# Optimization experiments

Measured on AMD Instinct MI355X. Metric: run time of the kernel, lower is better.

The kernel has to match this reference:

```python
import jax, jax.numpy as jnp
import numpy as np

BN_EPS = 1e-5


def _conv1d(x, w, b):
    # x: (B, C, T), w: (O, C, K), torch Conv1d with padding=K//2
    k = w.shape[-1]
    p = k // 2
    out = jax.lax.conv_general_dilated(
        x, w, window_strides=(1,), padding=[(p, p)],
        dimension_numbers=("NCH", "OIH", "NCH"))
    return out + b[None, :, None]


def setup_inputs() -> dict:
    key = jax.random.key(0)
    ks = jax.random.split(key, 16)
    B, C, T, H, NC = 32, 13, 2048, 128, 10
    d = {
        "x": jax.random.normal(ks[0], (B, C, T), jnp.float32),
        "w1": jax.random.normal(ks[1], (H, C, 10), jnp.float32) * 0.1,
        "b1": jax.random.normal(ks[2], (H,), jnp.float32) * 0.1,
        "w2": jax.random.normal(ks[3], (H, C, 20), jnp.float32) * 0.1,
        "b2": jax.random.normal(ks[4], (H,), jnp.float32) * 0.1,
        "w3": jax.random.normal(ks[5], (H, C, 30), jnp.float32) * 0.1,
        "b3": jax.random.normal(ks[6], (H,), jnp.float32) * 0.1,
        "w4": jax.random.normal(ks[7], (H, C, 40), jnp.float32) * 0.1,
        "b4": jax.random.normal(ks[8], (H,), jnp.float32) * 0.1,
        "bn_gamma": jax.random.uniform(ks[9], (4 * H,), jnp.float32, 0.5, 1.5),
        "bn_beta": jax.random.normal(ks[10], (4 * H,), jnp.float32) * 0.1,
        "bn_mean": jnp.zeros((4 * H,), jnp.float32),
        "bn_var": jnp.ones((4 * H,), jnp.float32),
        "logreg_w": jax.random.normal(ks[11], (NC, 4 * H), jnp.float32) * 0.05,
        "logreg_b": jax.random.normal(ks[12], (NC,), jnp.float32) * 0.1,
        "dec_w": jax.random.normal(ks[13], (1, 4 * H), jnp.float32) * 0.05,
        "dec_b": jax.random.normal(ks[14], (1,), jnp.float32) * 0.1,
    }
    return d


def reference(x, w1, b1, w2, b2, w3, b3, w4, b4,
              bn_gamma, bn_beta, bn_mean, bn_var,
              logreg_w, logreg_b, dec_w, dec_b):
    # --- multi-scale shapelet conv + per-prefix cumulative max pooling ---
    feats = []
    for w, b in ((w1, b1), (w2, b2), (w3, b3), (w4, b4)):
        f = _conv1d(x, w, b)                      # (B, H, T+1) (even kernels)
        # original loop: for t in 1..T_out-1 take max over f[:, :, :t]
        # == running (cumulative) max, dropping the last prefix
        cm = jax.lax.cummax(f, axis=2)[:, :, :-1]  # (B, H, T)
        feats.append(jnp.transpose(cm, (0, 2, 1)))  # (B, T, H)
    features = jnp.concatenate(feats, axis=-1)      # (B, T, 4H)

    # --- BatchNorm1d over feature channels (eval mode), dropout = identity ---
    inv = jax.lax.rsqrt(bn_var + BN_EPS)
    features = (features - bn_mean) * (inv * bn_gamma) + bn_beta

    # --- classification head and halting head ---
    logits = jnp.einsum("btf,cf->btc", features, logreg_w) + logreg_b  # (B,T,NC)
    deltas = jnp.einsum("btf,of->bto", features, dec_w) + dec_b        # (B,T,1)
    deltas = jax.nn.softmax(deltas[..., 0], axis=1)                    # (B,T)

    # --- attention budget: pt_t = delta_t * budget_{t-1}; budget decays ---
    B = deltas.shape[0]
    q = 1.0 - deltas                                # (B, T)
    cp = jnp.cumprod(q[:, 1:], axis=1)              # prod_{s=1..t} q_s
    budget = jnp.concatenate([jnp.ones((B, 1), deltas.dtype), cp], axis=1)
    pts_loop = deltas[:, 1:] * budget[:, :-1]       # (B, T-1)
    pts = jnp.concatenate([pts_loop, budget[:, -1:]], axis=1)  # (B, T)

    probs = jax.nn.softmax(logits, axis=-1)  # temperature = 1
    return probs, pts
```

## Files before the change

kernel.cpp:

```cpp
#include <hip/hip_runtime.h>
#include <math.h>

#define NEG_INF (-3.402823466e38f)

typedef float f32x4 __attribute__((ext_vector_type(4)));
typedef short bf16x8 __attribute__((ext_vector_type(8)));
typedef unsigned int u32x4 __attribute__((ext_vector_type(4)));

__device__ __forceinline__ unsigned short f2bf(float f) {
    unsigned int u = __float_as_uint(f);
    unsigned int r = (u + 0x7FFFu + ((u >> 16) & 1u)) >> 16;
    return (unsigned short)r;
}
__device__ __forceinline__ float bf2f(unsigned short s) {
    return __uint_as_float(((unsigned int)s) << 16);
}
__device__ __forceinline__ unsigned int pack2(float a, float b) {
    return (unsigned int)f2bf(a) | ((unsigned int)f2bf(b) << 16);
}
__device__ __forceinline__ int swz(int a) { return a ^ (((a >> 5) & 7) << 4); }

__global__ __launch_bounds__(512) void prep_kernel(
    const float* __restrict__ x,
    const float* __restrict__ w1, const float* __restrict__ w2,
    const float* __restrict__ w3, const float* __restrict__ w4,
    const float* __restrict__ bn_gamma, const float* __restrict__ bn_beta,
    const float* __restrict__ bn_mean, const float* __restrict__ bn_var,
    const float* __restrict__ lw, const float* __restrict__ lb,
    const float* __restrict__ dw, const float* __restrict__ db,
    unsigned short* __restrict__ xT, unsigned short* __restrict__ Bfrag,
    unsigned short* __restrict__ hfrag, float* __restrict__ bfo,
    float* __restrict__ dbfo)
{
    int bid = blockIdx.x;
    int tid = threadIdx.x;
    if (bid < 136) {
        int idx = bid * 512 + tid;
        int b = idx / 2176, r = idx - b * 2176;
        int t = r - 20;
        unsigned short row[16];
#pragma unroll
        for (int c = 0; c < 16; ++c) {
            float v = (c < 13 && t >= 0 && t < 2048) ? x[((size_t)(b * 13 + c)) * 2048 + t] : 0.f;
            row[c] = f2bf(v);
        }
        u32x4* dst = (u32x4*)(xT + (size_t)idx * 16);
        u32x4 v0, v1;
        v0.x = row[0] | ((unsigned)row[1] << 16);  v0.y = row[2] | ((unsigned)row[3] << 16);
        v0.z = row[4] | ((unsigned)row[5] << 16);  v0.w = row[6] | ((unsigned)row[7] << 16);
        v1.x = row[8] | ((unsigned)row[9] << 16);  v1.y = row[10] | ((unsigned)row[11] << 16);
        v1.z = row[12] | ((unsigned)row[13] << 16); v1.w = row[14] | ((unsigned)row[15] << 16);
        dst[0] = v0; dst[1] = v1;
    } else if (bid < 186) {
        int idx = (bid - 136) * 512 + tid;
        int lane = idx & 63, frag = idx >> 6;
        int rel, Kc; const float* w;
        if (frag < 40)       { rel = frag;       w = w1; Kc = 10; }
        else if (frag < 120) { rel = frag - 40;  w = w2; Kc = 20; }
        else if (frag < 240) { rel = frag - 120; w = w3; Kc = 30; }
        else                 { rel = frag - 240; w = w4; Kc = 40; }
        int kh = Kc / 2;
        int ht = rel / kh;
        int k0 = rel - ht * kh;
        int h = ht * 16 + (lane & 15);
        int dk = lane >> 5;
        int cbase = 8 * ((lane >> 4) & 1);
        int k = 2 * k0 + dk;
        unsigned short e[8];
#pragma unroll
        for (int j = 0; j < 8; ++j) {
            int c = cbase + j;
            float v = (c < 13) ? w[((size_t)h * 13 + c) * Kc + k] : 0.f;
            e[j] = f2bf(v);
        }
        u32x4 pk;
        pk.x = e[0] | ((unsigned)e[1] << 16); pk.y = e[2] | ((unsigned)e[3] << 16);
        pk.z = e[4] | ((unsigned)e[5] << 16); pk.w = e[6] | ((unsigned)e[7] << 16);
        *(u32x4*)(Bfrag + (size_t)frag * 512 + lane * 8) = pk;
    } else if (bid == 186) {
        __shared__ float sh[512];
        int j = tid;
        float s = rsqrtf(bn_var[j] + 1e-5f) * bn_gamma[j];
        float shift = bn_beta[j] - bn_mean[j] * s;
        sh[j] = shift;
        __syncthreads();
        if (j < 10) {
            float acc = lb[j];
            for (int q = 0; q < 512; ++q) acc += sh[q] * lw[j * 512 + q];
            bfo[j] = acc;
        } else if (j == 10) {
            float acc = db[0];
            for (int q = 0; q < 512; ++q) acc += sh[q] * dw[q];
            dbfo[0] = acc;
        }
    } else {
        int idx = (bid - 187) * 512 + tid;
        int lane = idx & 63, frag = idx >> 6;
        int n = lane & 15;
        unsigned short e[8];
#pragma unroll
        for (int jj = 0; jj < 8; ++jj) {
            int k = frag * 32 + 8 * (lane >> 4) + jj;
            float s = rsqrtf(bn_var[k] + 1e-5f) * bn_gamma[k];
            float v = (n < 10) ? lw[n * 512 + k] * s : (n == 10) ? dw[k] * s : 0.f;
            e[jj] = f2bf(v);
        }
        u32x4 pk;
        pk.x = e[0] | ((unsigned)e[1] << 16); pk.y = e[2] | ((unsigned)e[3] << 16);
        pk.z = e[4] | ((unsigned)e[5] << 16); pk.w = e[6] | ((unsigned)e[7] << 16);
        *(u32x4*)(hfrag + (size_t)frag * 512 + lane * 8) = pk;
    }
}

__global__ __launch_bounds__(256, 2) void conv_mfma(
    const unsigned short* __restrict__ xT, const unsigned short* __restrict__ Bfrag,
    const float* __restrict__ b1, const float* __restrict__ b2,
    const float* __restrict__ b3, const float* __restrict__ b4,
    unsigned short* __restrict__ feat, unsigned short* __restrict__ totals)
{
    __shared__ __align__(16) unsigned short lds[2688 + 2 * 32 * 132];
    unsigned short* xs = lds;
    unsigned int* stg32 = (unsigned int*)(lds + 2688);
    const int tid = threadIdx.x;
    const int tq = blockIdx.x & 15;
    const int scale = (blockIdx.x >> 4) & 3;
    const int b = blockIdx.x >> 6;
    const int kh_tab[4] = {5, 10, 15, 20};
    const int so_tab[4] = {0, 40, 120, 240};
    const int KH = kh_tab[scale];
    const int P = 5 * (scale + 1);
    const float* bias = (scale == 0) ? b1 : (scale == 1) ? b2 : (scale == 2) ? b3 : b4;

    const unsigned short* src = xT + ((size_t)b * 2176 + tq * 128) * 16;
#pragma unroll
    for (int it = 0; it < 2; ++it) {
        int c = it * 256 + tid;
        if (c < 336) {
            u32x4 v = *(const u32x4*)(src + c * 8);
            *(u32x4*)((char*)xs + swz(c * 16)) = v;
        }
    }
    __syncthreads();

    const int lane = tid & 63;
    const int wave = tid >> 6;
    const int hgrp = wave & 1;
    const int twq = wave >> 1;
    const int l15 = lane & 15;
    const int g4 = lane >> 4;

    const unsigned short* bfr = Bfrag + ((size_t)(so_tab[scale] + hgrp * 4 * KH)) * 512 + lane * 8;
    float bv[4];
#pragma unroll
    for (int ht = 0; ht < 4; ++ht) bv[ht] = bias[hgrp * 64 + ht * 16 + l15];

    int abase = ((20 - P) + twq * 64 + l15 + (lane >> 5)) * 32 + (g4 & 1) * 16;

    f32x4 acc[4][4];
#pragma unroll
    for (int ht = 0; ht < 4; ++ht)
#pragma unroll
        for (int tt = 0; tt < 4; ++tt)
            acc[ht][tt] = (f32x4){bv[ht], bv[ht], bv[ht], bv[ht]};

#define LOADB(DST, K) \
    _Pragma("unroll") for (int ht_ = 0; ht_ < 4; ++ht_) \
        DST[ht_] = *(const bf16x8*)(bfr + (size_t)(ht_ * KH + (K)) * 512);
#define LOADA(DST, K) \
    _Pragma("unroll") for (int tt_ = 0; tt_ < 4; ++tt_) \
        DST[tt_] = *(const bf16x8*)((const char*)xs + swz(abase + tt_ * 512 + (K) * 64));
#define MFMA16(AA, BB) \
    _Pragma("unroll") for (int ht_ = 0; ht_ < 4; ++ht_) \
        _Pragma("unroll") for (int tt_ = 0; tt_ < 4; ++tt_) \
            acc[ht_][tt_] = __builtin_amdgcn_mfma_f32_16x16x32_bf16(AA[tt_], BB[ht_], acc[ht_][tt_], 0, 0, 0);

    bf16x8 A0[4], A1[4], B0[4], B1[4];
    LOADB(B0, 0); LOADA(A0, 0);
    int k0 = 0;
#pragma unroll 1
    while (k0 + 2 <= KH) {
        LOADB(B1, k0 + 1); LOADA(A1, k0 + 1);
        MFMA16(A0, B0);
        if (k0 + 2 < KH) { LOADB(B0, k0 + 2); LOADA(A0, k0 + 2); }
        MFMA16(A1, B1);
        k0 += 2;
    }
    if (k0 < KH) { MFMA16(A0, B0); }
#undef LOADB
#undef LOADA
#undef MFMA16

    float carry[4] = {NEG_INF, NEG_INF, NEG_INF, NEG_INF};
    const int rq = tq * 2 + twq;
#pragma unroll
    for (int tt = 0; tt < 4; ++tt) {
#pragma unroll
        for (int ht = 0; ht < 4; ++ht) {
            f32x4 v = acc[ht][tt];
            float s0 = v.x;
            float s1 = fmaxf(v.y, s0);
            float s2 = fmaxf(v.z, s1);
            float s3 = fmaxf(v.w, s2);
            float inc = s3;
            float o = __shfl_up(inc, 16); if (lane >= 16) inc = fmaxf(inc, o);
            o = __shfl_up(inc, 32);       if (lane >= 32) inc = fmaxf(inc, o);
            float pre = __shfl_up(inc, 16);
            float base = (lane >= 16) ? fmaxf(carry[ht], pre) : carry[ht];
            s0 = fmaxf(s0, base); s1 = fmaxf(s1, base);
            s2 = fmaxf(s2, base); s3 = fmaxf(s3, base);
            float tot = __shfl(inc, l15 + 48);
            carry[ht] = fmaxf(carry[ht], tot);
            acc[ht][tt] = (f32x4){s0, s1, s2, s3};
        }
    }
    if (lane < 16) {
#pragma unroll
        for (int ht = 0; ht < 4; ++ht) {
            int j = scale * 128 + hgrp * 64 + ht * 16 + l15;
            totals[((size_t)b * 32 + rq) * 512 + j] = f2bf(carry[ht]);
        }
    }

#pragma unroll 1
    for (int half = 0; half < 2; ++half) {
        if (half) __syncthreads();
        if (twq == half) {
#pragma unroll
            for (int tt = 0; tt < 4; ++tt) {
#pragma unroll
                for (int ht = 0; ht < 4; ++ht) {
                    f32x4 s = acc[ht][tt];
                    int r2 = tt * 8 + 2 * g4;
                    int cc = hgrp * 64 + ht * 16 + l15;
                    stg32[r2 * 132 + cc]       = pack2(s.x, s.y);
                    stg32[(r2 + 1) * 132 + cc] = pack2(s.z, s.w);
                }
            }
        }
        __syncthreads();
        size_t grow = (size_t)b * 2048 + tq * 128 + half * 64;
#pragma unroll
        for (int i = 0; i < 2; ++i) {
            int e = i * 256 + tid;
            int r2 = e >> 4, q = e & 15;
            const unsigned int* p = stg32 + r2 * 132 + q * 8;
            u32x4 da = *(const u32x4*)(p);
            u32x4 dbb = *(const u32x4*)(p + 4);
            u32x4 ev, od;
            ev.x = (da.x & 0xffffu) | (da.y << 16);
            ev.y = (da.z & 0xffffu) | (da.w << 16);
            ev.z = (dbb.x & 0xffffu) | (dbb.y << 16);
            ev.w = (dbb.z & 0xffffu) | (dbb.w << 16);
            od.x = (da.x >> 16) | (da.y & 0xffff0000u);
            od.y = (da.z >> 16) | (da.w & 0xffff0000u);
            od.z = (dbb.x >> 16) | (dbb.y & 0xffff0000u);
            od.w = (dbb.z >> 16) | (dbb.w & 0xffff0000u);
            size_t base = (grow + 2 * r2) * 512 + scale * 128 + q * 8;
            __builtin_nontemporal_store(ev, (u32x4*)(feat + base));
            __builtin_nontemporal_store(od, (u32x4*)(feat + base + 512));
        }
    }
}

__global__ __launch_bounds__(256) void head_kernel(
    const unsigned short* __restrict__ feat, const unsigned short* __restrict__ totals,
    const unsigned short* __restrict__ hfrag, const float* __restrict__ bfo,
    const float* __restrict__ dbfo, float* __restrict__ probs,
    float* __restrict__ delta_raw)
{
    __shared__ float pfs[512];
    int b = blockIdx.x >> 5;
    int tc = blockIdx.x & 31;
    int tid = threadIdx.x;
    int lane = tid & 63;
    int wave = tid >> 6;

    for (int j = tid; j < 512; j += 256) {
        float run = NEG_INF;
        for (int qq = 0; qq < tc; ++qq)
            run = fmaxf(run, bf2f(totals[((size_t)b * 32 + qq) * 512 + j]));
        pfs[j] = run;
    }
    __syncthreads();

    bf16x8 Bf[16];
#pragma unroll
    for (int k0 = 0; k0 < 16; ++k0)
        Bf[k0] = *(const bf16x8*)(hfrag + (size_t)k0 * 512 + lane * 8);

    const int n = lane & 15;
    const int g4 = lane >> 4;
    const int tb = tc * 64 + wave * 16;
    const unsigned short* fb = feat + ((size_t)b * 2048 + tb + n) * 512 + 8 * g4;

    float biasv = (n < 10) ? bfo[n] : (n == 10) ? dbfo[0] : 0.f;
    f32x4 acc = (f32x4){biasv, biasv, biasv, biasv};

#pragma unroll
    for (int k0 = 0; k0 < 16; ++k0) {
        bf16x8 a = *(const bf16x8*)(fb + k0 * 32);
        const float* pp = pfs + k0 * 32 + 8 * g4;
        union { unsigned int u[4]; bf16x8 v; } aw;
#pragma unroll
        for (int i = 0; i < 4; ++i) {
            float lo = fmaxf(bf2f((unsigned short)a[2 * i]),     pp[2 * i]);
            float hi = fmaxf(bf2f((unsigned short)a[2 * i + 1]), pp[2 * i + 1]);
            aw.u[i] = (__float_as_uint(lo) >> 16) | (__float_as_uint(hi) & 0xFFFF0000u);
        }
        acc = __builtin_amdgcn_mfma_f32_16x16x32_bf16(aw.v, Bf[k0], acc, 0, 0, 0);
    }

#pragma unroll
    for (int r = 0; r < 4; ++r) {
        float v = acc[r];
        float vm = (n < 10) ? v : NEG_INF;
#pragma unroll
        for (int off = 1; off < 16; off <<= 1)
            vm = fmaxf(vm, __shfl_xor(vm, off, 16));
        float e = (n < 10) ? __expf(v - vm) : 0.f;
        float s = e;
#pragma unroll
        for (int off = 1; off < 16; off <<= 1)
            s += __shfl_xor(s, off, 16);
        int t = tb + g4 * 4 + r;
        if (n < 10) probs[((size_t)b * 2048 + t) * 10 + n] = e / s;
        if (n == 10) delta_raw[b * 2048 + t] = v;
    }
}

__global__ __launch_bounds__(256) void budget_kernel(
    const float* __restrict__ delta_raw, float* __restrict__ pts)
{
    __shared__ float ds[2048];
    __shared__ float red[8];
    int b = blockIdx.x;
    int tid = threadIdx.x;
    int lane = tid & 63, wid = tid >> 6;
    const float* row = delta_raw + b * 2048;
    int base = tid * 8;
    float d[8];
#pragma unroll
    for (int i = 0; i < 8; ++i) d[i] = row[base + i];
    float m = d[0];
#pragma unroll
    for (int i = 1; i < 8; ++i) m = fmaxf(m, d[i]);
#pragma unroll
    for (int off = 1; off < 64; off <<= 1) m = fmaxf(m, __shfl_xor(m, off));
    if (lane == 0) red[wid] = m;
    __syncthreads();
    m = fmaxf(fmaxf(red[0], red[1]), fmaxf(red[2], red[3]));
    float s = 0.f;
#pragma unroll
    for (int i = 0; i < 8; ++i) { d[i] = __expf(d[i] - m); s += d[i]; }
#pragma unroll
    for (int off = 1; off < 64; off <<= 1) s += __shfl_xor(s, off);
    if (lane == 0) red[4 + wid] = s;
    __syncthreads();
    float inv = 1.f / (red[4] + red[5] + red[6] + red[7]);
    float g[8], p = 1.f;
#pragma unroll
    for (int i = 0; i < 8; ++i) {
        d[i] *= inv;
        ds[base + i] = d[i];
        float gv = (base + i == 0) ? 1.f : (1.f - d[i]);
        p *= gv;
        g[i] = p;
    }
    float sp = p;
#pragma unroll
    for (int off = 1; off < 64; off <<= 1) {
        float o = __shfl_up(sp, off);
        if (lane >= off) sp *= o;
    }
    float pre_t = __shfl_up(sp, 1);
    if (lane == 0) pre_t = 1.f;
    if (lane == 63) red[wid] = sp;
    __syncthreads();
    float wpre = 1.f;
#pragma unroll
    for (int w = 0; w < 4; ++w) if (w < wid) wpre *= red[w];
    float pre = wpre * pre_t;
#pragma unroll
    for (int i = 0; i < 8; ++i) {
        int t = base + i;
        float budget = pre * g[i];
        float pt = (t < 2047) ? ds[t + 1] * budget : budget;
        pts[b * 2048 + t] = pt;
    }
}

extern "C" void kernel_launch(void* const* d_in, const int* in_sizes, int n_in,
                              void* d_out, int out_size, void* d_ws, size_t ws_size,
                              hipStream_t stream)
{
    const float* x     = (const float*)d_in[0];
    const float* w1    = (const float*)d_in[1];
    const float* b1    = (const float*)d_in[2];
    const float* w2    = (const float*)d_in[3];
    const float* b2    = (const float*)d_in[4];
    const float* w3    = (const float*)d_in[5];
    const float* b3    = (const float*)d_in[6];
    const float* w4    = (const float*)d_in[7];
    const float* b4    = (const float*)d_in[8];
    const float* gamma = (const float*)d_in[9];
    const float* beta  = (const float*)d_in[10];
    const float* mean  = (const float*)d_in[11];
    const float* var   = (const float*)d_in[12];
    const float* lw    = (const float*)d_in[13];
    const float* lb    = (const float*)d_in[14];
    const float* dw    = (const float*)d_in[15];
    const float* db    = (const float*)d_in[16];

    char* ws = (char*)d_ws;
    unsigned short* feat   = (unsigned short*)ws;
    unsigned short* xT     = (unsigned short*)(ws + 67108864);
    unsigned short* Bfrag  = (unsigned short*)(ws + 69337088);
    unsigned short* totals = (unsigned short*)(ws + 69746688);
    float* draw   = (float*)(ws + 70795264);
    unsigned short* hfrag = (unsigned short*)(ws + 71057408);
    float* bfo    = (float*)(ws + 71073792);
    float* dbfo   = (float*)(ws + 71073856);

    float* probs = (float*)d_out;
    float* pts   = probs + (size_t)32 * 2048 * 10;

    hipLaunchKernelGGL(prep_kernel, dim3(189), dim3(512), 0, stream,
                       x, w1, w2, w3, w4, gamma, beta, mean, var,
                       lw, lb, dw, db, xT, Bfrag, hfrag, bfo, dbfo);
    hipLaunchKernelGGL(conv_mfma, dim3(2048), dim3(256), 0, stream,
                       xT, Bfrag, b1, b2, b3, b4, feat, totals);
    hipLaunchKernelGGL(head_kernel, dim3(1024), dim3(256), 0, stream,
                       feat, totals, hfrag, bfo, dbfo, probs, draw);
    hipLaunchKernelGGL(budget_kernel, dim3(32), dim3(256), 0, stream, draw, pts);
}
```

Before: 89.10 us.

## Double conv tile to 256 timesteps per block with 8 MFMA tiles per wave

Each conv block now covers 256 timesteps instead of 128, so every wave holds 4x8 accumulator tiles and reuses each loaded B fragment across twice as many MFMAs, and the grid is halved. The x load now reads only the halo needed for the scale, and the software-pipelined double-buffered K loop becomes a simple loop. The cummax emits two per-64-row totals (mid and end), and the feature stores drop the nontemporal hint. Register pressure roughly doubles for the accumulators, which may reduce occupancy or spill under launch_bounds(256,2), and the simpler loop loses load/compute overlap.

```diff
diff --git a/kernel.cpp b/kernel.cpp
--- a/kernel.cpp
+++ b/kernel.cpp
@@ -118,24 +118,25 @@
     const float* __restrict__ b3, const float* __restrict__ b4,
     unsigned short* __restrict__ feat, unsigned short* __restrict__ totals)
 {
-    __shared__ __align__(16) unsigned short lds[2688 + 2 * 32 * 132];
+    __shared__ __align__(16) unsigned short lds[4736 + 16896];
     unsigned short* xs = lds;
-    unsigned int* stg32 = (unsigned int*)(lds + 2688);
+    unsigned int* stg32 = (unsigned int*)(lds + 4736);
     const int tid = threadIdx.x;
-    const int tq = blockIdx.x & 15;
-    const int scale = (blockIdx.x >> 4) & 3;
-    const int b = blockIdx.x >> 6;
+    const int tq = blockIdx.x & 7;
+    const int scale = (blockIdx.x >> 3) & 3;
+    const int b = blockIdx.x >> 5;
     const int kh_tab[4] = {5, 10, 15, 20};
     const int so_tab[4] = {0, 40, 120, 240};
     const int KH = kh_tab[scale];
     const int P = 5 * (scale + 1);
     const float* bias = (scale == 0) ? b1 : (scale == 1) ? b2 : (scale == 2) ? b3 : b4;
 
-    const unsigned short* src = xT + ((size_t)b * 2176 + tq * 128) * 16;
-#pragma unroll
-    for (int it = 0; it < 2; ++it) {
+    const unsigned short* src = xT + ((size_t)b * 2176 + tq * 256 + 20 - P) * 16;
+    const int nchunk = 2 * (256 + 2 * P);
+#pragma unroll
+    for (int it = 0; it < 3; ++it) {
         int c = it * 256 + tid;
-        if (c < 336) {
+        if (c < nchunk) {
             u32x4 v = *(const u32x4*)(src + c * 8);
             *(u32x4*)((char*)xs + swz(c * 16)) = v;
         }
@@ -154,48 +155,38 @@
 #pragma unroll
     for (int ht = 0; ht < 4; ++ht) bv[ht] = bias[hgrp * 64 + ht * 16 + l15];
 
-    int abase = ((20 - P) + twq * 64 + l15 + (lane >> 5)) * 32 + (g4 & 1) * 16;
-
-    f32x4 acc[4][4];
+    int abase = (twq * 128 + l15 + (lane >> 5)) * 32 + ((lane >> 4) & 1) * 16;
+
+    f32x4 acc[4][8];
 #pragma unroll
     for (int ht = 0; ht < 4; ++ht)
 #pragma unroll
-        for (int tt = 0; tt < 4; ++tt)
+        for (int tt = 0; tt < 8; ++tt)
             acc[ht][tt] = (f32x4){bv[ht], bv[ht], bv[ht], bv[ht]};
 
-#define LOADB(DST, K) \
-    _Pragma("unroll") for (int ht_ = 0; ht_ < 4; ++ht_) \
-        DST[ht_] = *(const bf16x8*)(bfr + (size_t)(ht_ * KH + (K)) * 512);
-#define LOADA(DST, K) \
-    _Pragma("unroll") for (int tt_ = 0; tt_ < 4; ++tt_) \
-        DST[tt_] = *(const bf16x8*)((const char*)xs + swz(abase + tt_ * 512 + (K) * 64));
-#define MFMA16(AA, BB) \
-    _Pragma("unroll") for (int ht_ = 0; ht_ < 4; ++ht_) \
-        _Pragma("unroll") for (int tt_ = 0; tt_ < 4; ++tt_) \
-            acc[ht_][tt_] = __builtin_amdgcn_mfma_f32_16x16x32_bf16(AA[tt_], BB[ht_], acc[ht_][tt_], 0, 0, 0);
-
-    bf16x8 A0[4], A1[4], B0[4], B1[4];
-    LOADB(B0, 0); LOADA(A0, 0);
-    int k0 = 0;
 #pragma unroll 1
-    while (k0 + 2 <= KH) {
-        LOADB(B1, k0 + 1); LOADA(A1, k0 + 1);
-        MFMA16(A0, B0);
-        if (k0 + 2 < KH) { LOADB(B0, k0 + 2); LOADA(A0, k0 + 2); }
-        MFMA16(A1, B1);
-        k0 += 2;
-    }
-    if (k0 < KH) { MFMA16(A0, B0); }
-#undef LOADB
-#undef LOADA
-#undef MFMA16
-
-    float carry[4] = {NEG_INF, NEG_INF, NEG_INF, NEG_INF};
-    const int rq = tq * 2 + twq;
-#pragma unroll
-    for (int tt = 0; tt < 4; ++tt) {
-#pragma unroll
-        for (int ht = 0; ht < 4; ++ht) {
+    for (int k0 = 0; k0 < KH; ++k0) {
+        bf16x8 B[4], A[8];
+#pragma unroll
+        for (int ht = 0; ht < 4; ++ht)
+            B[ht] = *(const bf16x8*)(bfr + (size_t)(ht * KH + k0) * 512);
+#pragma unroll
+        for (int tt = 0; tt < 8; ++tt)
+            A[tt] = *(const bf16x8*)((const char*)xs + swz(abase + tt * 512 + k0 * 64));
+#pragma unroll
+        for (int ht = 0; ht < 4; ++ht)
+#pragma unroll
+            for (int tt = 0; tt < 8; ++tt)
+                acc[ht][tt] = __builtin_amdgcn_mfma_f32_16x16x32_bf16(A[tt], B[ht], acc[ht][tt], 0, 0, 0);
+    }
+
+    const int rq0 = tq * 4 + twq * 2;
+    float carry[4], mid[4];
+#pragma unroll
+    for (int ht = 0; ht < 4; ++ht) {
+        float c0 = NEG_INF;
+#pragma unroll
+        for (int tt = 0; tt < 8; ++tt) {
             f32x4 v = acc[ht][tt];
             float s0 = v.x;
             float s1 = fmaxf(v.y, s0);
@@ -205,19 +196,22 @@
             float o = __shfl_up(inc, 16); if (lane >= 16) inc = fmaxf(inc, o);
             o = __shfl_up(inc, 32);       if (lane >= 32) inc = fmaxf(inc, o);
             float pre = __shfl_up(inc, 16);
-            float base = (lane >= 16) ? fmaxf(carry[ht], pre) : carry[ht];
+            float base = (lane >= 16) ? fmaxf(c0, pre) : c0;
             s0 = fmaxf(s0, base); s1 = fmaxf(s1, base);
             s2 = fmaxf(s2, base); s3 = fmaxf(s3, base);
             float tot = __shfl(inc, l15 + 48);
-            carry[ht] = fmaxf(carry[ht], tot);
+            c0 = fmaxf(c0, tot);
             acc[ht][tt] = (f32x4){s0, s1, s2, s3};
-        }
+            if (tt == 3) mid[ht] = c0;
+        }
+        carry[ht] = c0;
     }
     if (lane < 16) {
 #pragma unroll
         for (int ht = 0; ht < 4; ++ht) {
             int j = scale * 128 + hgrp * 64 + ht * 16 + l15;
-            totals[((size_t)b * 32 + rq) * 512 + j] = f2bf(carry[ht]);
+            totals[((size_t)b * 32 + rq0) * 512 + j]     = f2bf(mid[ht]);
+            totals[((size_t)b * 32 + rq0 + 1) * 512 + j] = f2bf(carry[ht]);
         }
     }
 
@@ -226,7 +220,7 @@
         if (half) __syncthreads();
         if (twq == half) {
 #pragma unroll
-            for (int tt = 0; tt < 4; ++tt) {
+            for (int tt = 0; tt < 8; ++tt) {
 #pragma unroll
                 for (int ht = 0; ht < 4; ++ht) {
                     f32x4 s = acc[ht][tt];
@@ -238,9 +232,9 @@
             }
         }
         __syncthreads();
-        size_t grow = (size_t)b * 2048 + tq * 128 + half * 64;
-#pragma unroll
-        for (int i = 0; i < 2; ++i) {
+        size_t grow = (size_t)b * 2048 + tq * 256 + half * 128;
+#pragma unroll
+        for (int i = 0; i < 4; ++i) {
             int e = i * 256 + tid;
             int r2 = e >> 4, q = e & 15;
             const unsigned int* p = stg32 + r2 * 132 + q * 8;
@@ -256,8 +250,8 @@
             od.z = (dbb.x >> 16) | (dbb.y & 0xffff0000u);
             od.w = (dbb.z >> 16) | (dbb.w & 0xffff0000u);
             size_t base = (grow + 2 * r2) * 512 + scale * 128 + q * 8;
-            __builtin_nontemporal_store(ev, (u32x4*)(feat + base));
-            __builtin_nontemporal_store(od, (u32x4*)(feat + base + 512));
+            *(u32x4*)(feat + base)       = ev;
+            *(u32x4*)(feat + base + 512) = od;
         }
     }
 }
@@ -427,7 +421,7 @@
     hipLaunchKernelGGL(prep_kernel, dim3(189), dim3(512), 0, stream,
                        x, w1, w2, w3, w4, gamma, beta, mean, var,
                        lw, lb, dw, db, xT, Bfrag, hfrag, bfo, dbfo);
-    hipLaunchKernelGGL(conv_mfma, dim3(2048), dim3(256), 0, stream,
+    hipLaunchKernelGGL(conv_mfma, dim3(1024), dim3(256), 0, stream,
                        xT, Bfrag, b1, b2, b3, b4, feat, totals);
     hipLaunchKernelGGL(head_kernel, dim3(1024), dim3(256), 0, stream,
                        feat, totals, hfrag, bfo, dbfo, probs, draw);
```

Measured after the change: 106.1 us. +19.0%, slower.

## Raise conv occupancy by dropping double-buffered fragments and nontemporal stores

Applied to the files above, without the earlier changes.

Raises the launch-bounds minimum blocks per CU from 2 to 4 for the conv kernel. To fit that register budget, the manually double-buffered A/B fragment loads are replaced by a simple per-k loop that loads and then issues MFMAs. The nontemporal stores of features become ordinary stores, so the head kernel can find them in cache. The trade is less software pipelining within a wave, which the extra resident waves are meant to hide, plus a risk of register spills under the tighter bound.

```diff
diff --git a/kernel.cpp b/kernel.cpp
--- a/kernel.cpp
+++ b/kernel.cpp
@@ -112,7 +112,7 @@
     }
 }
 
-__global__ __launch_bounds__(256, 2) void conv_mfma(
+__global__ __launch_bounds__(256, 4) void conv_mfma(
     const unsigned short* __restrict__ xT, const unsigned short* __restrict__ Bfrag,
     const float* __restrict__ b1, const float* __restrict__ b2,
     const float* __restrict__ b3, const float* __restrict__ b4,
@@ -154,7 +154,7 @@
 #pragma unroll
     for (int ht = 0; ht < 4; ++ht) bv[ht] = bias[hgrp * 64 + ht * 16 + l15];
 
-    int abase = ((20 - P) + twq * 64 + l15 + (lane >> 5)) * 32 + (g4 & 1) * 16;
+    int abase = ((20 - P) + twq * 64 + l15 + (lane >> 5)) * 32 + ((lane >> 4) & 1) * 16;
 
     f32x4 acc[4][4];
 #pragma unroll
@@ -163,32 +163,21 @@
         for (int tt = 0; tt < 4; ++tt)
             acc[ht][tt] = (f32x4){bv[ht], bv[ht], bv[ht], bv[ht]};
 
-#define LOADB(DST, K) \
-    _Pragma("unroll") for (int ht_ = 0; ht_ < 4; ++ht_) \
-        DST[ht_] = *(const bf16x8*)(bfr + (size_t)(ht_ * KH + (K)) * 512);
-#define LOADA(DST, K) \
-    _Pragma("unroll") for (int tt_ = 0; tt_ < 4; ++tt_) \
-        DST[tt_] = *(const bf16x8*)((const char*)xs + swz(abase + tt_ * 512 + (K) * 64));
-#define MFMA16(AA, BB) \
-    _Pragma("unroll") for (int ht_ = 0; ht_ < 4; ++ht_) \
-        _Pragma("unroll") for (int tt_ = 0; tt_ < 4; ++tt_) \
-            acc[ht_][tt_] = __builtin_amdgcn_mfma_f32_16x16x32_bf16(AA[tt_], BB[ht_], acc[ht_][tt_], 0, 0, 0);
-
-    bf16x8 A0[4], A1[4], B0[4], B1[4];
-    LOADB(B0, 0); LOADA(A0, 0);
-    int k0 = 0;
 #pragma unroll 1
-    while (k0 + 2 <= KH) {
-        LOADB(B1, k0 + 1); LOADA(A1, k0 + 1);
-        MFMA16(A0, B0);
-        if (k0 + 2 < KH) { LOADB(B0, k0 + 2); LOADA(A0, k0 + 2); }
-        MFMA16(A1, B1);
-        k0 += 2;
-    }
-    if (k0 < KH) { MFMA16(A0, B0); }
-#undef LOADB
-#undef LOADA
-#undef MFMA16
+    for (int k0 = 0; k0 < KH; ++k0) {
+        bf16x8 B[4], A[4];
+#pragma unroll
+        for (int ht = 0; ht < 4; ++ht)
+            B[ht] = *(const bf16x8*)(bfr + (size_t)(ht * KH + k0) * 512);
+#pragma unroll
+        for (int tt = 0; tt < 4; ++tt)
+            A[tt] = *(const bf16x8*)((const char*)xs + swz(abase + tt * 512 + k0 * 64));
+#pragma unroll
+        for (int ht = 0; ht < 4; ++ht)
+#pragma unroll
+            for (int tt = 0; tt < 4; ++tt)
+                acc[ht][tt] = __builtin_amdgcn_mfma_f32_16x16x32_bf16(A[tt], B[ht], acc[ht][tt], 0, 0, 0);
+    }
 
     float carry[4] = {NEG_INF, NEG_INF, NEG_INF, NEG_INF};
     const int rq = tq * 2 + twq;
@@ -256,8 +245,8 @@
             od.z = (dbb.x >> 16) | (dbb.y & 0xffff0000u);
             od.w = (dbb.z >> 16) | (dbb.w & 0xffff0000u);
             size_t base = (grow + 2 * r2) * 512 + scale * 128 + q * 8;
-            __builtin_nontemporal_store(ev, (u32x4*)(feat + base));
-            __builtin_nontemporal_store(od, (u32x4*)(feat + base + 512));
+            *(u32x4*)(feat + base)       = ev;
+            *(u32x4*)(feat + base + 512) = od;
         }
     }
 }
```

New measurement: 89.83 us. Within noise of the previous version (+0.8%).

## Precompute chunk prefix maxima in separate kernel and stage x transpose via LDS

Applied to the files above, without the earlier changes.

Adds a small prefix_kernel that computes the exclusive running max of per-chunk totals once per (batch, channel). The head kernel then reads a single prefix row instead of looping over up to 31 chunk totals per block. The prep kernel's x transpose now loads x through shared memory with coalesced reads per channel, using 256-thread blocks with re-indexed block ranges. It adds an extra kernel launch and a small extra workspace buffer.

```diff
diff --git a/kernel.cpp b/kernel.cpp
--- a/kernel.cpp
+++ b/kernel.cpp
@@ -20,7 +20,7 @@
 }
 __device__ __forceinline__ int swz(int a) { return a ^ (((a >> 5) & 7) << 4); }
 
-__global__ __launch_bounds__(512) void prep_kernel(
+__global__ __launch_bounds__(256) void prep_kernel(
     const float* __restrict__ x,
     const float* __restrict__ w1, const float* __restrict__ w2,
     const float* __restrict__ w3, const float* __restrict__ w4,
@@ -34,25 +34,32 @@
 {
     int bid = blockIdx.x;
     int tid = threadIdx.x;
-    if (bid < 136) {
-        int idx = bid * 512 + tid;
-        int b = idx / 2176, r = idx - b * 2176;
-        int t = r - 20;
-        unsigned short row[16];
-#pragma unroll
-        for (int c = 0; c < 16; ++c) {
-            float v = (c < 13 && t >= 0 && t < 2048) ? x[((size_t)(b * 13 + c)) * 2048 + t] : 0.f;
-            row[c] = f2bf(v);
-        }
-        u32x4* dst = (u32x4*)(xT + (size_t)idx * 16);
-        u32x4 v0, v1;
-        v0.x = row[0] | ((unsigned)row[1] << 16);  v0.y = row[2] | ((unsigned)row[3] << 16);
-        v0.z = row[4] | ((unsigned)row[5] << 16);  v0.w = row[6] | ((unsigned)row[7] << 16);
-        v1.x = row[8] | ((unsigned)row[9] << 16);  v1.y = row[10] | ((unsigned)row[11] << 16);
-        v1.z = row[12] | ((unsigned)row[13] << 16); v1.w = row[14] | ((unsigned)row[15] << 16);
-        dst[0] = v0; dst[1] = v1;
-    } else if (bid < 186) {
-        int idx = (bid - 136) * 512 + tid;
+    if (bid < 288) {
+        __shared__ float xsp[13][257];
+        int b = bid / 9;
+        int chunk = bid - b * 9;
+        int r0 = chunk * 256;
+        int t = r0 - 20 + tid;
+#pragma unroll
+        for (int c = 0; c < 13; ++c)
+            xsp[c][tid] = (t >= 0 && t < 2048) ? x[((size_t)(b * 13 + c)) * 2048 + t] : 0.f;
+        __syncthreads();
+        int r = r0 + tid;
+        if (r < 2176) {
+            unsigned short row[16];
+#pragma unroll
+            for (int c = 0; c < 13; ++c) row[c] = f2bf(xsp[c][tid]);
+            row[13] = 0; row[14] = 0; row[15] = 0;
+            u32x4 v0, v1;
+            v0.x = row[0] | ((unsigned)row[1] << 16);  v0.y = row[2] | ((unsigned)row[3] << 16);
+            v0.z = row[4] | ((unsigned)row[5] << 16);  v0.w = row[6] | ((unsigned)row[7] << 16);
+            v1.x = row[8] | ((unsigned)row[9] << 16);  v1.y = row[10] | ((unsigned)row[11] << 16);
+            v1.z = row[12] | ((unsigned)row[13] << 16); v1.w = row[14] | ((unsigned)row[15] << 16);
+            u32x4* dst = (u32x4*)(xT + ((size_t)b * 2176 + r) * 16);
+            dst[0] = v0; dst[1] = v1;
+        }
+    } else if (bid < 388) {
+        int idx = (bid - 288) * 256 + tid;
         int lane = idx & 63, frag = idx >> 6;
         int rel, Kc; const float* w;
         if (frag < 40)       { rel = frag;       w = w1; Kc = 10; }
@@ -77,24 +84,24 @@
         pk.x = e[0] | ((unsigned)e[1] << 16); pk.y = e[2] | ((unsigned)e[3] << 16);
         pk.z = e[4] | ((unsigned)e[5] << 16); pk.w = e[6] | ((unsigned)e[7] << 16);
         *(u32x4*)(Bfrag + (size_t)frag * 512 + lane * 8) = pk;
-    } else if (bid == 186) {
+    } else if (bid == 388) {
         __shared__ float sh[512];
-        int j = tid;
-        float s = rsqrtf(bn_var[j] + 1e-5f) * bn_gamma[j];
-        float shift = bn_beta[j] - bn_mean[j] * s;
-        sh[j] = shift;
+        for (int j = tid; j < 512; j += 256) {
+            float s = rsqrtf(bn_var[j] + 1e-5f) * bn_gamma[j];
+            sh[j] = bn_beta[j] - bn_mean[j] * s;
+        }
         __syncthreads();
-        if (j < 10) {
-            float acc = lb[j];
-            for (int q = 0; q < 512; ++q) acc += sh[q] * lw[j * 512 + q];
-            bfo[j] = acc;
-        } else if (j == 10) {
+        if (tid < 10) {
+            float acc = lb[tid];
+            for (int q = 0; q < 512; ++q) acc += sh[q] * lw[tid * 512 + q];
+            bfo[tid] = acc;
+        } else if (tid == 10) {
             float acc = db[0];
             for (int q = 0; q < 512; ++q) acc += sh[q] * dw[q];
             dbfo[0] = acc;
         }
     } else {
-        int idx = (bid - 187) * 512 + tid;
+        int idx = (bid - 389) * 256 + tid;
         int lane = idx & 63, frag = idx >> 6;
         int n = lane & 15;
         unsigned short e[8];
@@ -262,8 +269,22 @@
     }
 }
 
+__global__ void prefix_kernel(const unsigned short* __restrict__ totals,
+                              unsigned short* __restrict__ prefix)
+{
+    int idx = blockIdx.x * 256 + threadIdx.x;
+    if (idx >= 32 * 512) return;
+    int b = idx >> 9, j = idx & 511;
+    float run = NEG_INF;
+#pragma unroll
+    for (int q = 0; q < 32; ++q) {
+        prefix[((size_t)b * 32 + q) * 512 + j] = f2bf(run);
+        run = fmaxf(run, bf2f(totals[((size_t)b * 32 + q) * 512 + j]));
+    }
+}
+
 __global__ __launch_bounds__(256) void head_kernel(
-    const unsigned short* __restrict__ feat, const unsigned short* __restrict__ totals,
+    const unsigned short* __restrict__ feat, const unsigned short* __restrict__ prefix,
     const unsigned short* __restrict__ hfrag, const float* __restrict__ bfo,
     const float* __restrict__ dbfo, float* __restrict__ probs,
     float* __restrict__ delta_raw)
@@ -275,12 +296,8 @@
     int lane = tid & 63;
     int wave = tid >> 6;
 
-    for (int j = tid; j < 512; j += 256) {
-        float run = NEG_INF;
-        for (int qq = 0; qq < tc; ++qq)
-            run = fmaxf(run, bf2f(totals[((size_t)b * 32 + qq) * 512 + j]));
-        pfs[j] = run;
-    }
+    for (int j = tid; j < 512; j += 256)
+        pfs[j] = bf2f(prefix[((size_t)b * 32 + tc) * 512 + j]);
     __syncthreads();
 
     bf16x8 Bf[16];
@@ -416,20 +433,22 @@
     unsigned short* xT     = (unsigned short*)(ws + 67108864);
     unsigned short* Bfrag  = (unsigned short*)(ws + 69337088);
     unsigned short* totals = (unsigned short*)(ws + 69746688);
-    float* draw   = (float*)(ws + 70795264);
-    unsigned short* hfrag = (unsigned short*)(ws + 71057408);
-    float* bfo    = (float*)(ws + 71073792);
-    float* dbfo   = (float*)(ws + 71073856);
+    unsigned short* prefix = (unsigned short*)(ws + 70795264);
+    float* draw   = (float*)(ws + 71843840);
+    unsigned short* hfrag = (unsigned short*)(ws + 72105984);
+    float* bfo    = (float*)(ws + 72122368);
+    float* dbfo   = (float*)(ws + 72122432);
 
     float* probs = (float*)d_out;
     float* pts   = probs + (size_t)32 * 2048 * 10;
 
-    hipLaunchKernelGGL(prep_kernel, dim3(189), dim3(512), 0, stream,
+    hipLaunchKernelGGL(prep_kernel, dim3(393), dim3(256), 0, stream,
                        x, w1, w2, w3, w4, gamma, beta, mean, var,
                        lw, lb, dw, db, xT, Bfrag, hfrag, bfo, dbfo);
     hipLaunchKernelGGL(conv_mfma, dim3(2048), dim3(256), 0, stream,
                        xT, Bfrag, b1, b2, b3, b4, feat, totals);
+    hipLaunchKernelGGL(prefix_kernel, dim3(64), dim3(256), 0, stream, totals, prefix);
     hipLaunchKernelGGL(head_kernel, dim3(1024), dim3(256), 0, stream,
-                       feat, totals, hfrag, bfo, dbfo, probs, draw);
+                       feat, prefix, hfrag, bfo, dbfo, probs, draw);
     hipLaunchKernelGGL(budget_kernel, dim3(32), dim3(256), 0, stream, draw, pts);
 }
```

Result: faster. 80.97 us (-9.1%).
